# Kernel optimization log

Hardware: AMD Instinct MI355X
Metric: run time of the kernel (lower is better)

The kernel has to match this reference:

```python
import jax, jax.numpy as jnp
import numpy as np

B, S, D = 4, 2048, 1024


def setup_inputs() -> dict:
    key = jax.random.key(0)
    ks = jax.random.split(key, 7)
    s = 1.0 / np.sqrt(D)
    return {
        "x": jax.random.normal(ks[0], (B, S, D), dtype=jnp.float32),
        "Wq": jax.random.normal(ks[1], (D, D), dtype=jnp.float32) * s,
        "bq": jax.random.normal(ks[2], (D,), dtype=jnp.float32) * 0.01,
        "Wk": jax.random.normal(ks[3], (D, D), dtype=jnp.float32) * s,
        "bk": jax.random.normal(ks[4], (D,), dtype=jnp.float32) * 0.01,
        "Wv": jax.random.normal(ks[5], (D, D), dtype=jnp.float32) * s,
        "bv": jax.random.normal(ks[6], (D,), dtype=jnp.float32) * 0.01,
    }


def reference(x, Wq, bq, Wk, bk, Wv, bv):
    # x: [B, S, D]; Linear uses y = x @ W^T + b (torch convention)
    q = jnp.einsum("bsd,ed->bse", x, Wq) + bq
    k = jnp.einsum("bsd,ed->bse", x, Wk) + bk
    v = jnp.einsum("bsd,ed->bse", x, Wv) + bv
    # NOTE: original module applies softmax(q k^T) with NO 1/sqrt(d) scaling
    scores = jnp.einsum("bqd,bkd->bqk", q, k)  # [B, S, S]
    attn = jax.nn.softmax(scores, axis=-1)
    return jnp.einsum("bqk,bkd->bqd", attn, v)  # [B, S, D]
```

## Files before the change

### kernel.cpp

```cpp
#include <hip/hip_runtime.h>


#define Bb 4
#define Ss 2048
#define Dd 1024
#define Mtot 8192

typedef __bf16 bf16x8 __attribute__((ext_vector_type(8)));
typedef _Float16 f16x8 __attribute__((ext_vector_type(8)));
typedef float f32x4 __attribute__((ext_vector_type(4)));
typedef int i32x4 __attribute__((ext_vector_type(4)));
typedef signed char i8x16 __attribute__((ext_vector_type(16)));
typedef unsigned short u16;
typedef unsigned int u32;
typedef unsigned char u8;
typedef u16 u16x8 __attribute__((ext_vector_type(8)));
typedef u16 u16x4 __attribute__((ext_vector_type(4)));
typedef void __attribute__((address_space(1))) gvoid_t;
typedef void __attribute__((address_space(3))) svoid_t;

#define XC 0.0625f
#define XCI 16.f
#define XFI 4096.f
#define WC 1.953125e-3f
#define WCI 512.f
#define WFI 131072.f
#define W1S 7.62939453125e-6f
#define SM_P 1.220703125e-4f
#define SX_P 4.76837158203125e-7f
#define SY_P 1.862645149230957e-9f
#define S00 3.90625e-3f
#define S01 1.52587890625e-5f
#define S11 5.9604644775390625e-8f
#define SG00 3.814697265625e-6f
#define SG01 1.4901161193847656e-8f
#define SG11 5.820766091346741e-11f

__device__ __forceinline__ void gl_lds16(const void* g, void* l) {
  __builtin_amdgcn_global_load_lds((gvoid_t*)g, (svoid_t*)l, 16, 0, 0);
}

__device__ __forceinline__ u16 f2bf(float f) {
  u32 u = __builtin_bit_cast(u32, f);
  u = (u + 0x7FFFu + ((u >> 16) & 1u)) >> 16;
  return (u16)u;
}
__device__ __forceinline__ u16 f2h(float f) {
  return __builtin_bit_cast(u16, (_Float16)f);
}
__device__ __forceinline__ bf16x8 frag_ld(const char* p) {
  u16x8 v = *(const u16x8*)p;
  return __builtin_bit_cast(bf16x8, v);
}
__device__ __forceinline__ f16x8 frag_ld_h(const char* p) {
  u16x8 v = *(const u16x8*)p;
  return __builtin_bit_cast(f16x8, v);
}
__device__ __forceinline__ f32x4 mfma_bf16(bf16x8 a, bf16x8 b, f32x4 c) {
  return __builtin_amdgcn_mfma_f32_16x16x32_bf16(a, b, c, 0, 0, 0);
}
__device__ __forceinline__ i32x4 mfma_i8(i32x4 a, i32x4 b, i32x4 c) {
  return __builtin_amdgcn_mfma_i32_16x16x64_i8(a, b, c, 0, 0, 0);
}
__device__ __forceinline__ void dig2(float v, float cs, float ci, float fi,
                                     int& d0, int& d1) {
  float t = fminf(fmaxf(v * ci, -127.f), 127.f);
  d0 = __float2int_rn(t);
  float res = v - (float)d0 * cs;
  float u = fminf(fmaxf(res * fi, -127.f), 127.f);
  d1 = __float2int_rn(u);
}

template <int GX, int GY, int GZ>
__device__ __forceinline__ void xcd_swz(int& bx, int& by, int& bz) {
  constexpr int N = GX * GY * GZ;
  int flat = (int)blockIdx.x + GX * ((int)blockIdx.y + GY * (int)blockIdx.z);
  int s = (flat & 7) * (N >> 3) + (flat >> 3);
  bx = s & (GX - 1);
  by = (s / GX) & (GY - 1);
  bz = s / (GX * GY);
}

__device__ __forceinline__ void wait_bar_keep8() {
  asm volatile("s_waitcnt vmcnt(8)" ::: "memory");
  __builtin_amdgcn_s_barrier();
  __builtin_amdgcn_sched_barrier(0);
}
__device__ __forceinline__ void wait_bar_drain() {
  asm volatile("s_waitcnt vmcnt(0)" ::: "memory");
  __builtin_amdgcn_s_barrier();
  __builtin_amdgcn_sched_barrier(0);
}
__device__ __forceinline__ void end_bar() {
  __builtin_amdgcn_sched_barrier(0);
  __builtin_amdgcn_s_barrier();
}

template <int ROUNDS, int C>
__device__ __forceinline__ void stageF(const char* g, long row0, long ldb,
                                       long k0b, char* l, int tid) {
#pragma unroll
  for (int r = 0; r < ROUNDS; ++r) {
    int s = r * 256 + tid;
    int sub = s / (16 * C);
    int t = s % (16 * C);
    int h = t >> 6;
    int lk = (t >> 4) & 3;
    int lr = t & 15;
    gl_lds16(g + (row0 + sub * 16 + lr) * ldb + k0b + (h * 4 + lk) * 16,
             l + s * 16);
  }
}

__global__ void __launch_bounds__(256) convert_w(
    const float* __restrict__ Wq, const float* __restrict__ Wk,
    const float* __restrict__ Wv,
    u8* __restrict__ wq0, u8* __restrict__ wq1,
    u8* __restrict__ wk0, u8* __restrict__ wk1, u16* __restrict__ wvh) {
  long b = blockIdx.x;
  if (b < 2048) {
    int which = (int)(b >> 10);
    const float* src = which ? Wk : Wq;
    u8* o0 = which ? wk0 : wq0;
    u8* o1 = which ? wk1 : wq1;
    long i = (b & 1023) * 256 + threadIdx.x;
    f32x4 v = ((const f32x4*)src)[i];
    u32 p0 = 0, p1 = 0;
#pragma unroll
    for (int j = 0; j < 4; ++j) {
      int d0, d1;
      dig2(v[j], WC, WCI, WFI, d0, d1);
      p0 |= ((u32)(d0 & 255)) << (8 * j);
      p1 |= ((u32)(d1 & 255)) << (8 * j);
    }
    ((u32*)o0)[i] = p0;
    ((u32*)o1)[i] = p1;
  } else {
    long i = (b - 2048) * 256 + threadIdx.x;
    f32x4 v = ((const f32x4*)Wv)[i];
    u16x4 h;
#pragma unroll
    for (int j = 0; j < 4; ++j) h[j] = f2bf(v[j]);
    ((u16x4*)wvh)[i] = h;
  }
}

__global__ void __launch_bounds__(256) transpose_w(
    const u8* __restrict__ wq0, const u8* __restrict__ wq1,
    const u8* __restrict__ wk0, const u8* __restrict__ wk1,
    u8* __restrict__ wqT0, u8* __restrict__ wqT1,
    u8* __restrict__ wkT0, u8* __restrict__ wkT1) {
  __shared__ u8 T[64][68];
  int a = blockIdx.z;
  const u8* src = a == 0 ? wq0 : a == 1 ? wq1 : a == 2 ? wk0 : wk1;
  u8* dst = a == 0 ? wqT0 : a == 1 ? wqT1 : a == 2 ? wkT0 : wkT1;
  int bi = blockIdx.y, bj = blockIdx.x;
  int t = threadIdx.x, r = t >> 2, c4 = t & 3;
  const u32* s = (const u32*)(src + (long)(bi * 64 + r) * 1024 + bj * 64 + c4 * 16);
  u32 v0 = s[0], v1 = s[1], v2 = s[2], v3 = s[3];
  u32* trow = (u32*)&T[r][c4 * 16];
  trow[0] = v0; trow[1] = v1; trow[2] = v2; trow[3] = v3;
  __syncthreads();
  u32 o[4] = {0, 0, 0, 0};
#pragma unroll
  for (int j = 0; j < 16; ++j)
    o[j >> 2] |= ((u32)T[c4 * 16 + j][r]) << (8 * (j & 3));
  u32* d = (u32*)(dst + (long)(bj * 64 + r) * 1024 + bi * 64 + c4 * 16);
  d[0] = o[0]; d[1] = o[1]; d[2] = o[2]; d[3] = o[3];
}

__global__ void __launch_bounds__(256) gvec_kernel(
    const u8* __restrict__ wqT0, const u8* __restrict__ wqT1,
    const u8* __restrict__ wkT0, const u8* __restrict__ wkT1,
    const float* __restrict__ bq, const float* __restrict__ bk,
    float* __restrict__ gq, float* __restrict__ gk, float* __restrict__ cbuf) {
  __shared__ float sbq[1024], sbk[1024];
  int tid = threadIdx.x;
  ((f32x4*)sbq)[tid] = ((const f32x4*)bq)[tid];
  ((f32x4*)sbk)[tid] = ((const f32x4*)bk)[tid];
  __syncthreads();
  int wave = tid >> 6, lane = tid & 63;
#pragma unroll
  for (int rr = 0; rr < 2; ++rr) {
    int d = blockIdx.x * 8 + wave * 2 + rr;
    i8x16 a0 = *(const i8x16*)(wqT0 + (long)d * 1024 + lane * 16);
    i8x16 a1 = *(const i8x16*)(wqT1 + (long)d * 1024 + lane * 16);
    i8x16 c0 = *(const i8x16*)(wkT0 + (long)d * 1024 + lane * 16);
    i8x16 c1 = *(const i8x16*)(wkT1 + (long)d * 1024 + lane * 16);
    float sq = 0.f, sk = 0.f;
#pragma unroll
    for (int j = 0; j < 16; ++j) {
      sq += ((float)a0[j] * WC + (float)a1[j] * W1S) * sbk[lane * 16 + j];
      sk += ((float)c0[j] * WC + (float)c1[j] * W1S) * sbq[lane * 16 + j];
    }
#pragma unroll
    for (int off = 32; off >= 1; off >>= 1) {
      sq += __shfl_xor(sq, off);
      sk += __shfl_xor(sk, off);
    }
    if (!lane) { gq[d] = sq; gk[d] = sk; }
  }
  if (blockIdx.x == 0 && wave == 0) {
    float c = 0.f;
#pragma unroll
    for (int j = 0; j < 16; ++j) c += sbq[lane * 16 + j] * sbk[lane * 16 + j];
#pragma unroll
    for (int off = 32; off >= 1; off >>= 1) c += __shfl_xor(c, off);
    if (!lane) cbuf[0] = c;
  }
}

__global__ void __launch_bounds__(256) convert_x(
    const float* __restrict__ x, const float* __restrict__ gq,
    const float* __restrict__ gk, const float* __restrict__ cbuf,
    u16* __restrict__ xh, u8* __restrict__ xd0, u8* __restrict__ xd1,
    float* __restrict__ ubuf, float* __restrict__ wbuf) {
  long b = blockIdx.x;
  int tid = threadIdx.x;
  long i = b * 256 + tid;
  f32x4 v = ((const f32x4*)x)[i];
  u16x4 h;
  u32 p0 = 0, p1 = 0;
#pragma unroll
  for (int j = 0; j < 4; ++j) {
    h[j] = f2bf(v[j]);
    int d0, d1;
    dig2(v[j], XC, XCI, XFI, d0, d1);
    p0 |= ((u32)(d0 & 255)) << (8 * j);
    p1 |= ((u32)(d1 & 255)) << (8 * j);
  }
  ((u16x4*)xh)[i] = h;
  ((u32*)xd0)[i] = p0;
  ((u32*)xd1)[i] = p1;

  f32x4 g4 = ((const f32x4*)gq)[tid];
  f32x4 k4 = ((const f32x4*)gk)[tid];
  float pu = v[0] * g4[0] + v[1] * g4[1] + v[2] * g4[2] + v[3] * g4[3];
  float pw = v[0] * k4[0] + v[1] * k4[1] + v[2] * k4[2] + v[3] * k4[3];
#pragma unroll
  for (int off = 32; off >= 1; off >>= 1) {
    pu += __shfl_xor(pu, off);
    pw += __shfl_xor(pw, off);
  }
  __shared__ float ru[4], rw[4];
  int wave = tid >> 6, lane = tid & 63;
  if (!lane) { ru[wave] = pu; rw[wave] = pw; }
  __syncthreads();
  if (!tid) {
    ubuf[b] = ru[0] + ru[1] + ru[2] + ru[3] + cbuf[0];
    wbuf[b] = rw[0] + rw[1] + rw[2] + rw[3];
  }
}

__global__ void __launch_bounds__(256, 2) g_part(
    const u8* __restrict__ wqT0, const u8* __restrict__ wqT1,
    const u8* __restrict__ wkT0, const u8* __restrict__ wkT1,
    float* __restrict__ Gpart) {
  __shared__ char lds[65536];
  const int tid = threadIdx.x;
  const int bx = blockIdx.x, by = blockIdx.y, bz = blockIdx.z;
  const long m0 = (long)by * 128;
  const int n0 = bx * 128;
  const int k00 = bz * 256;
  const int wave = tid >> 6, lane = tid & 63;
  const int wm = wave >> 1, wn = wave & 1;
  const int lr = lane & 15, lk = lane >> 4;

  i32x4 accM[4][4] = {};
  i32x4 accX[4][4] = {};
  i32x4 accY[4][4] = {};

  auto stage = [&](char* L, int kk) {
    stageF<2, 4>((const char*)wqT0, m0, 1024, kk, L + 0, tid);
    stageF<2, 4>((const char*)wqT1, m0, 1024, kk, L + 8192, tid);
    stageF<2, 4>((const char*)wkT0, n0, 1024, kk, L + 16384, tid);
    stageF<2, 4>((const char*)wkT1, n0, 1024, kk, L + 24576, tid);
  };
  auto compute = [&](const char* L) {
    i32x4 b0[4], b1[4];
#pragma unroll
    for (int nt = 0; nt < 4; ++nt) {
      int rb = (wn * 4 + nt) * 1024 + lane * 16;
      b0[nt] = *(const i32x4*)(L + 16384 + rb);
      b1[nt] = *(const i32x4*)(L + 24576 + rb);
    }
    __builtin_amdgcn_s_setprio(1);
#pragma unroll
    for (int mt = 0; mt < 4; ++mt) {
      int ra = (wm * 4 + mt) * 1024 + lane * 16;
      i32x4 a0 = *(const i32x4*)(L + ra);
      i32x4 a1 = *(const i32x4*)(L + 8192 + ra);
#pragma unroll
      for (int nt = 0; nt < 4; ++nt) {
        accM[mt][nt] = mfma_i8(a0, b0[nt], accM[mt][nt]);
        accX[mt][nt] = mfma_i8(a0, b1[nt], accX[mt][nt]);
        accX[mt][nt] = mfma_i8(a1, b0[nt], accX[mt][nt]);
        accY[mt][nt] = mfma_i8(a1, b1[nt], accY[mt][nt]);
      }
    }
    __builtin_amdgcn_s_setprio(0);
  };

  stage(lds, k00);
  for (int t = 0; t < 3; ++t) {
    char* L = lds + (t & 1) * 32768;
    stage(lds + ((t + 1) & 1) * 32768, k00 + (t + 1) * 64);
    wait_bar_keep8();
    compute(L);
    end_bar();
  }
  {
    char* L = lds + 32768;
    wait_bar_drain();
    compute(L);
  }

#pragma unroll
  for (int mt = 0; mt < 4; ++mt)
#pragma unroll
    for (int nt = 0; nt < 4; ++nt) {
      int e = n0 + wn * 64 + nt * 16 + lr;
      int gmb = (int)m0 + wm * 64 + mt * 16 + lk * 4;
      f32x4 o;
#pragma unroll
      for (int r = 0; r < 4; ++r)
        o[r] = (float)accM[mt][nt][r] * SG00 + (float)accX[mt][nt][r] * SG01 +
               (float)accY[mt][nt][r] * SG11;
      *(f32x4*)(Gpart + ((long)bz << 20) + (long)e * 1024 + gmb) = o;
    }
}

__global__ void __launch_bounds__(256) g_reduce(const float* __restrict__ Gpart,
                                                u8* __restrict__ Gt0,
                                                u8* __restrict__ Gt1) {
  int n = blockIdx.x, tid = threadIdx.x;
  long o = (long)n * 1024 + tid * 4;
  f32x4 v = *(const f32x4*)(Gpart + o);
  f32x4 v1 = *(const f32x4*)(Gpart + (1L << 20) + o);
  f32x4 v2 = *(const f32x4*)(Gpart + (2L << 20) + o);
  f32x4 v3 = *(const f32x4*)(Gpart + (3L << 20) + o);
#pragma unroll
  for (int j = 0; j < 4; ++j) v[j] = v[j] + v1[j] + v2[j] + v3[j];
  u32 p0 = 0, p1 = 0;
#pragma unroll
  for (int j = 0; j < 4; ++j) {
    int d0, d1;
    dig2(v[j], WC, WCI, WFI, d0, d1);
    p0 |= ((u32)(d0 & 255)) << (8 * j);
    p1 |= ((u32)(d1 & 255)) << (8 * j);
  }
  ((u32*)Gt0)[n * 256 + tid] = p0;
  ((u32*)Gt1)[n * 256 + tid] = p1;
}

__global__ void __launch_bounds__(256, 2) t_gemm(
    const u8* __restrict__ xd0, const u8* __restrict__ xd1,
    const u8* __restrict__ Gt0, const u8* __restrict__ Gt1,
    u8* __restrict__ t0, u8* __restrict__ t1) {
  __shared__ char lds[65536];
  const int tid = threadIdx.x;
  int bx, by, bz;
  xcd_swz<8, 64, 1>(bx, by, bz);
  const long m0 = (long)by * 128;
  const int n0 = bx * 128;
  const int wave = tid >> 6, lane = tid & 63;
  const int wm = wave >> 1, wn = wave & 1;
  const int lr = lane & 15, lk = lane >> 4;

  i32x4 accM[4][4] = {};
  i32x4 accX[4][4] = {};
  i32x4 accY[4][4] = {};

  auto stage = [&](char* L, int kk) {
    stageF<2, 4>((const char*)xd0, m0, Dd, kk, L + 0, tid);
    stageF<2, 4>((const char*)xd1, m0, Dd, kk, L + 8192, tid);
    stageF<2, 4>((const char*)Gt0, n0, 1024, kk, L + 16384, tid);
    stageF<2, 4>((const char*)Gt1, n0, 1024, kk, L + 24576, tid);
  };
  auto compute = [&](const char* L) {
    i32x4 b0[4], b1[4];
#pragma unroll
    for (int nt = 0; nt < 4; ++nt) {
      int rb = (wn * 4 + nt) * 1024 + lane * 16;
      b0[nt] = *(const i32x4*)(L + 16384 + rb);
      b1[nt] = *(const i32x4*)(L + 24576 + rb);
    }
    __builtin_amdgcn_s_setprio(1);
#pragma unroll
    for (int mt = 0; mt < 4; ++mt) {
      int ra = (wm * 4 + mt) * 1024 + lane * 16;
      i32x4 a0 = *(const i32x4*)(L + ra);
      i32x4 a1 = *(const i32x4*)(L + 8192 + ra);
#pragma unroll
      for (int nt = 0; nt < 4; ++nt) {
        accM[mt][nt] = mfma_i8(a0, b0[nt], accM[mt][nt]);
        accX[mt][nt] = mfma_i8(a0, b1[nt], accX[mt][nt]);
        accX[mt][nt] = mfma_i8(a1, b0[nt], accX[mt][nt]);
        accY[mt][nt] = mfma_i8(a1, b1[nt], accY[mt][nt]);
      }
    }
    __builtin_amdgcn_s_setprio(0);
  };

  stage(lds, 0);
  for (int t = 0; t < Dd / 64 - 1; ++t) {
    char* L = lds + (t & 1) * 32768;
    stage(lds + ((t + 1) & 1) * 32768, (t + 1) * 64);
    wait_bar_keep8();
    compute(L);
    end_bar();
  }
  {
    char* L = lds + ((Dd / 64 - 1) & 1) * 32768;
    wait_bar_drain();
    compute(L);
  }

#pragma unroll
  for (int mt = 0; mt < 4; ++mt)
#pragma unroll
    for (int nt = 0; nt < 4; ++nt)
#pragma unroll
      for (int r = 0; r < 4; ++r) {
        long gm = m0 + wm * 64 + mt * 16 + lk * 4 + r;
        int e = n0 + wn * 64 + nt * 16 + lr;
        float v = (float)accM[mt][nt][r] * SM_P +
                  (float)accX[mt][nt][r] * SX_P +
                  (float)accY[mt][nt][r] * SY_P;
        int d0, d1;
        dig2(v, XC, XCI, XFI, d0, d1);
        long idx = gm * Dd + e;
        t0[idx] = (u8)d0;
        t1[idx] = (u8)d1;
      }
}

__global__ void __launch_bounds__(256) v_gemm(
    const u16* __restrict__ xh, const u16* __restrict__ wvh,
    const float* __restrict__ bv, u16* __restrict__ vt) {
  __shared__ char lds[65536];
  const int tid = threadIdx.x;
  int bx, by, bz;
  xcd_swz<8, 64, 1>(bx, by, bz);
  const long m0 = (long)by * 128;
  const int n0 = bx * 128;
  const int wave = tid >> 6, lane = tid & 63;
  const int wm = wave >> 1, wn = wave & 1;
  const int lr = lane & 15, lk = lane >> 4;

  f32x4 acc[4][4] = {};

  auto stage = [&](char* L, int k0) {
    stageF<4, 8>((const char*)xh, m0, (long)Dd * 2, (long)k0 * 2, L + 0, tid);
    stageF<4, 8>((const char*)wvh, n0, (long)Dd * 2, (long)k0 * 2, L + 16384, tid);
  };
  auto compute = [&](const char* L) {
    bf16x8 af[2][4], bfr[2][4];
#pragma unroll
    for (int ks = 0; ks < 2; ++ks)
#pragma unroll
      for (int i = 0; i < 4; ++i) {
        af[ks][i] = frag_ld(L + (wm * 4 + i) * 2048 + ks * 1024 + lane * 16);
        bfr[ks][i] = frag_ld(L + 16384 + (wn * 4 + i) * 2048 + ks * 1024 + lane * 16);
      }
    __builtin_amdgcn_s_setprio(1);
#pragma unroll
    for (int ks = 0; ks < 2; ++ks)
#pragma unroll
      for (int mt = 0; mt < 4; ++mt)
#pragma unroll
        for (int nt = 0; nt < 4; ++nt)
          acc[mt][nt] = mfma_bf16(af[ks][mt], bfr[ks][nt], acc[mt][nt]);
    __builtin_amdgcn_s_setprio(0);
  };

  stage(lds, 0);
  for (int t = 0; t < Dd / 64 - 1; ++t) {
    char* L = lds + (t & 1) * 32768;
    stage(lds + ((t + 1) & 1) * 32768, (t + 1) * 64);
    wait_bar_keep8();
    compute(L);
    end_bar();
  }
  {
    char* L = lds + ((Dd / 64 - 1) & 1) * 32768;
    wait_bar_drain();
    compute(L);
  }

#pragma unroll
  for (int mt = 0; mt < 4; ++mt)
#pragma unroll
    for (int nt = 0; nt < 4; ++nt)
#pragma unroll
      for (int r = 0; r < 4; ++r) {
        long gm = m0 + wm * 64 + mt * 16 + lk * 4 + r;
        int e = n0 + wn * 64 + nt * 16 + lr;
        float v = acc[mt][nt][r] + bv[e];
        long b = gm >> 11, s = gm & 2047;
        vt[(b * Dd + e) * (long)Ss + s] = f2h(v);
      }
}

__global__ void __launch_bounds__(256, 2) score_gemm(
    const u8* __restrict__ t0, const u8* __restrict__ t1,
    const u8* __restrict__ xd0, const u8* __restrict__ xd1,
    const float* __restrict__ ubuf, const float* __restrict__ wbuf,
    float* __restrict__ scores) {
  __shared__ char lds[65536];
  const int tid = threadIdx.x;
  int bx, by, bz;
  xcd_swz<16, 16, 4>(bx, by, bz);
  const int z = bz;
  const long base = (long)z * Ss * Dd;
  const long m0 = (long)by * 128;
  const int n0 = bx * 128;
  const int wave = tid >> 6, lane = tid & 63;
  const int wm = wave >> 1, wn = wave & 1;
  const int lr = lane & 15, lk = lane >> 4;

  i32x4 accM[4][4] = {};
  i32x4 accX[4][4] = {};
  i32x4 accY[4][4] = {};

  auto stage = [&](char* L, int kk) {
    stageF<2, 4>((const char*)t0 + base, m0, Dd, kk, L + 0, tid);
    stageF<2, 4>((const char*)t1 + base, m0, Dd, kk, L + 8192, tid);
    stageF<2, 4>((const char*)xd0 + base, n0, Dd, kk, L + 16384, tid);
    stageF<2, 4>((const char*)xd1 + base, n0, Dd, kk, L + 24576, tid);
  };
  auto compute = [&](const char* L) {
    i32x4 b0[4], b1[4];
#pragma unroll
    for (int nt = 0; nt < 4; ++nt) {
      int rb = (wn * 4 + nt) * 1024 + lane * 16;
      b0[nt] = *(const i32x4*)(L + 16384 + rb);
      b1[nt] = *(const i32x4*)(L + 24576 + rb);
    }
    __builtin_amdgcn_s_setprio(1);
#pragma unroll
    for (int mt = 0; mt < 4; ++mt) {
      int ra = (wm * 4 + mt) * 1024 + lane * 16;
      i32x4 a0 = *(const i32x4*)(L + ra);
      i32x4 a1 = *(const i32x4*)(L + 8192 + ra);
#pragma unroll
      for (int nt = 0; nt < 4; ++nt) {
        accM[mt][nt] = mfma_i8(a0, b0[nt], accM[mt][nt]);
        accX[mt][nt] = mfma_i8(a0, b1[nt], accX[mt][nt]);
        accX[mt][nt] = mfma_i8(a1, b0[nt], accX[mt][nt]);
        accY[mt][nt] = mfma_i8(a1, b1[nt], accY[mt][nt]);
      }
    }
    __builtin_amdgcn_s_setprio(0);
  };

  stage(lds, 0);
  for (int t = 0; t < Dd / 64 - 1; ++t) {
    char* L = lds + (t & 1) * 32768;
    stage(lds + ((t + 1) & 1) * 32768, (t + 1) * 64);
    wait_bar_keep8();
    compute(L);
    end_bar();
  }
  {
    char* L = lds + ((Dd / 64 - 1) & 1) * 32768;
    wait_bar_drain();
    compute(L);
  }

  float* srow = scores + (long)z * Ss * Ss;
#pragma unroll
  for (int mt = 0; mt < 4; ++mt)
#pragma unroll
    for (int nt = 0; nt < 4; ++nt)
#pragma unroll
      for (int r = 0; r < 4; ++r) {
        long i = m0 + wm * 64 + mt * 16 + lk * 4 + r;
        int j = n0 + wn * 64 + nt * 16 + lr;
        srow[i * Ss + j] = (float)accM[mt][nt][r] * S00 +
                           (float)accX[mt][nt][r] * S01 +
                           (float)accY[mt][nt][r] * S11 +
                           ubuf[(z << 11) + i] + wbuf[(z << 11) + j];
      }
}

__global__ void __launch_bounds__(256) softmax_rows(const float* __restrict__ scores,
                                                    u16* __restrict__ P) {
  const long r = blockIdx.x;
  const float* row = scores + r * Ss;
  u16* prow = P + r * Ss;
  const int t = threadIdx.x;
  const int wave = t >> 6, lane = t & 63;
  f32x4 v0 = ((const f32x4*)row)[t * 2];
  f32x4 v1 = ((const f32x4*)row)[t * 2 + 1];
  float a[8];
#pragma unroll
  for (int j = 0; j < 4; ++j) { a[j] = v0[j]; a[4 + j] = v1[j]; }

  float m = a[0];
#pragma unroll
  for (int j = 1; j < 8; ++j) m = fmaxf(m, a[j]);
#pragma unroll
  for (int off = 32; off >= 1; off >>= 1) m = fmaxf(m, __shfl_xor(m, off));
  __shared__ float red[4];
  if (lane == 0) red[wave] = m;
  __syncthreads();
  m = fmaxf(fmaxf(red[0], red[1]), fmaxf(red[2], red[3]));

  float e[8];
  float s = 0.f;
#pragma unroll
  for (int j = 0; j < 8; ++j) { e[j] = __expf(a[j] - m); s += e[j]; }
#pragma unroll
  for (int off = 32; off >= 1; off >>= 1) s += __shfl_xor(s, off);
  __syncthreads();
  if (lane == 0) red[wave] = s;
  __syncthreads();
  s = red[0] + red[1] + red[2] + red[3];
  float inv = 1.0f / s;

  u16x8 pk;
#pragma unroll
  for (int j = 0; j < 8; ++j) pk[j] = f2h(e[j] * inv);
  ((u16x8*)prow)[t] = pk;
}

__global__ void __launch_bounds__(256) pv_gemm(const u16* __restrict__ P,
                                               const u16* __restrict__ vt,
                                               float* __restrict__ out) {
  __shared__ char lds[65536];
  const int tid = threadIdx.x;
  int bx, by, bz;
  xcd_swz<8, 16, 4>(bx, by, bz);
  const int z = bz;
  const u16* A = P + (long)z * Ss * Ss;
  const u16* Bp = vt + (long)z * Dd * Ss;
  const long m0 = (long)by * 128;
  const int n0 = bx * 128;

  const int wave = tid >> 6, lane = tid & 63;
  const int wm = wave >> 1, wn = wave & 1;
  const int lr = lane & 15, lk = lane >> 4;

  f32x4 acc[4][4] = {};

  auto stage = [&](char* L, int k0) {
    stageF<4, 8>((const char*)A, m0, (long)Ss * 2, (long)k0 * 2, L + 0, tid);
    stageF<4, 8>((const char*)Bp, n0, (long)Ss * 2, (long)k0 * 2, L + 16384, tid);
  };
  auto compute = [&](const char* L) {
    f16x8 af[2][4], bfr[2][4];
#pragma unroll
    for (int ks = 0; ks < 2; ++ks)
#pragma unroll
      for (int i = 0; i < 4; ++i) {
        af[ks][i] = frag_ld_h(L + (wm * 4 + i) * 2048 + ks * 1024 + lane * 16);
        bfr[ks][i] = frag_ld_h(L + 16384 + (wn * 4 + i) * 2048 + ks * 1024 + lane * 16);
      }
    __builtin_amdgcn_s_setprio(1);
#pragma unroll
    for (int ks = 0; ks < 2; ++ks)
#pragma unroll
      for (int mt = 0; mt < 4; ++mt)
#pragma unroll
        for (int nt = 0; nt < 4; ++nt)
          acc[mt][nt] = __builtin_amdgcn_mfma_f32_16x16x32_f16(af[ks][mt], bfr[ks][nt], acc[mt][nt], 0, 0, 0);
    __builtin_amdgcn_s_setprio(0);
  };

  stage(lds, 0);
  for (int t = 0; t < Ss / 64 - 1; ++t) {
    char* L = lds + (t & 1) * 32768;
    stage(lds + ((t + 1) & 1) * 32768, (t + 1) * 64);
    wait_bar_keep8();
    compute(L);
    end_bar();
  }
  {
    char* L = lds + ((Ss / 64 - 1) & 1) * 32768;
    wait_bar_drain();
    compute(L);
  }

  float* orow = out + (long)z * Ss * Dd;
#pragma unroll
  for (int mt = 0; mt < 4; ++mt)
#pragma unroll
    for (int nt = 0; nt < 4; ++nt)
#pragma unroll
      for (int r = 0; r < 4; ++r) {
        long i = m0 + wm * 64 + mt * 16 + lk * 4 + r;
        int e = n0 + wn * 64 + nt * 16 + lr;
        orow[i * Dd + e] = acc[mt][nt][r];
      }
}

extern "C" void kernel_launch(void* const* d_in, const int* in_sizes, int n_in,
                              void* d_out, int out_size, void* d_ws, size_t ws_size,
                              hipStream_t stream) {
  const float* x = (const float*)d_in[0];
  const float* Wq = (const float*)d_in[1];
  const float* bq = (const float*)d_in[2];
  const float* Wk = (const float*)d_in[3];
  const float* bk = (const float*)d_in[4];
  const float* Wv = (const float*)d_in[5];
  const float* bv = (const float*)d_in[6];
  float* out = (float*)d_out;

  char* p = (char*)d_ws;
  float* scores = (float*)p;
  u16* xh = (u16*)p;
  u8* Gt0 = (u8*)p;
  u8* Gt1 = (u8*)(p + (1L << 20));
  u16* wvh = (u16*)(p + (16L << 20));
  u8* xd0 = (u8*)(p + (64L << 20));
  u8* xd1 = (u8*)(p + (72L << 20));
  u8* t0 = (u8*)(p + (80L << 20));
  u8* t1 = (u8*)(p + (88L << 20));
  u8* wq0 = (u8*)(p + (80L << 20));
  u8* wq1 = wq0 + (1L << 20);
  u8* wk0 = wq0 + (2L << 20);
  u8* wk1 = wq0 + (3L << 20);
  float* Gpart = (float*)(p + (80L << 20));
  u16* Pbuf = (u16*)(p + (96L << 20));
  u16* vt = (u16*)(p + (128L << 20));
  u8* wqT0 = (u8*)(p + (144L << 20));
  u8* wqT1 = wqT0 + (1L << 20);
  u8* wkT0 = wqT0 + (2L << 20);
  u8* wkT1 = wqT0 + (3L << 20);
  float* gq = (float*)(p + (148L << 20));
  float* gk = gq + 1024;
  float* ubuf = gq + 2048;
  float* wbuf = ubuf + 8192;
  float* cbuf = wbuf + 8192;

  convert_w<<<dim3(3072), dim3(256), 0, stream>>>(Wq, Wk, Wv, wq0, wq1, wk0, wk1, wvh);
  transpose_w<<<dim3(16, 16, 4), dim3(256), 0, stream>>>(
      wq0, wq1, wk0, wk1, wqT0, wqT1, wkT0, wkT1);
  gvec_kernel<<<dim3(128), dim3(256), 0, stream>>>(
      wqT0, wqT1, wkT0, wkT1, bq, bk, gq, gk, cbuf);
  convert_x<<<dim3(8192), dim3(256), 0, stream>>>(
      x, gq, gk, cbuf, xh, xd0, xd1, ubuf, wbuf);
  v_gemm<<<dim3(Dd / 128, Mtot / 128), dim3(256), 0, stream>>>(xh, wvh, bv, vt);
  g_part<<<dim3(8, 8, 4), dim3(256), 0, stream>>>(wqT0, wqT1, wkT0, wkT1, Gpart);
  g_reduce<<<dim3(1024), dim3(256), 0, stream>>>(Gpart, Gt0, Gt1);
  t_gemm<<<dim3(Dd / 128, Mtot / 128), dim3(256), 0, stream>>>(
      xd0, xd1, Gt0, Gt1, t0, t1);
  score_gemm<<<dim3(Ss / 128, Ss / 128, Bb), dim3(256), 0, stream>>>(
      t0, t1, xd0, xd1, ubuf, wbuf, scores);
  softmax_rows<<<dim3(Bb * Ss), dim3(256), 0, stream>>>(scores, Pbuf);
  pv_gemm<<<dim3(Dd / 128, Ss / 128, Bb), dim3(256), 0, stream>>>(Pbuf, vt, out);
}
```

Baseline: 359.4 us.

## Replace split-int8 score GEMM with single fp16 MFMA GEMM

The score GEMM used to multiply two-digit int8 splits of T and x, which took four int8 MFMAs per tile pair. It now stores T as fp16 and computes the scores with one fp16 MFMA per k-step. The x and Wv conversions and the V GEMM move from bf16 to fp16, and the xh buffer is relocated in the workspace. This cuts MFMA work and LDS staging in the score kernel. In exchange the score GEMM reads twice the bytes per element, and there is a precision risk because unscaled scores are sensitive to error in T.

```diff
diff --git a/kernel.cpp b/kernel.cpp
--- a/kernel.cpp
+++ b/kernel.cpp
@@ -6,7 +6,6 @@
 #define Dd 1024
 #define Mtot 8192
 
-typedef __bf16 bf16x8 __attribute__((ext_vector_type(8)));
 typedef _Float16 f16x8 __attribute__((ext_vector_type(8)));
 typedef float f32x4 __attribute__((ext_vector_type(4)));
 typedef int i32x4 __attribute__((ext_vector_type(4)));
@@ -29,9 +28,6 @@
 #define SM_P 1.220703125e-4f
 #define SX_P 4.76837158203125e-7f
 #define SY_P 1.862645149230957e-9f
-#define S00 3.90625e-3f
-#define S01 1.52587890625e-5f
-#define S11 5.9604644775390625e-8f
 #define SG00 3.814697265625e-6f
 #define SG01 1.4901161193847656e-8f
 #define SG11 5.820766091346741e-11f
@@ -40,24 +36,15 @@
   __builtin_amdgcn_global_load_lds((gvoid_t*)g, (svoid_t*)l, 16, 0, 0);
 }
 
-__device__ __forceinline__ u16 f2bf(float f) {
-  u32 u = __builtin_bit_cast(u32, f);
-  u = (u + 0x7FFFu + ((u >> 16) & 1u)) >> 16;
-  return (u16)u;
-}
 __device__ __forceinline__ u16 f2h(float f) {
   return __builtin_bit_cast(u16, (_Float16)f);
-}
-__device__ __forceinline__ bf16x8 frag_ld(const char* p) {
-  u16x8 v = *(const u16x8*)p;
-  return __builtin_bit_cast(bf16x8, v);
 }
 __device__ __forceinline__ f16x8 frag_ld_h(const char* p) {
   u16x8 v = *(const u16x8*)p;
   return __builtin_bit_cast(f16x8, v);
 }
-__device__ __forceinline__ f32x4 mfma_bf16(bf16x8 a, bf16x8 b, f32x4 c) {
-  return __builtin_amdgcn_mfma_f32_16x16x32_bf16(a, b, c, 0, 0, 0);
+__device__ __forceinline__ f32x4 mfma_f16(f16x8 a, f16x8 b, f32x4 c) {
+  return __builtin_amdgcn_mfma_f32_16x16x32_f16(a, b, c, 0, 0, 0);
 }
 __device__ __forceinline__ i32x4 mfma_i8(i32x4 a, i32x4 b, i32x4 c) {
   return __builtin_amdgcn_mfma_i32_16x16x64_i8(a, b, c, 0, 0, 0);
@@ -140,7 +127,7 @@
     f32x4 v = ((const f32x4*)Wv)[i];
     u16x4 h;
 #pragma unroll
-    for (int j = 0; j < 4; ++j) h[j] = f2bf(v[j]);
+    for (int j = 0; j < 4; ++j) h[j] = f2h(v[j]);
     ((u16x4*)wvh)[i] = h;
   }
 }
@@ -223,7 +210,7 @@
   u32 p0 = 0, p1 = 0;
 #pragma unroll
   for (int j = 0; j < 4; ++j) {
-    h[j] = f2bf(v[j]);
+    h[j] = f2h(v[j]);
     int d0, d1;
     dig2(v[j], XC, XCI, XFI, d0, d1);
     p0 |= ((u32)(d0 & 255)) << (8 * j);
@@ -356,7 +343,7 @@
 __global__ void __launch_bounds__(256, 2) t_gemm(
     const u8* __restrict__ xd0, const u8* __restrict__ xd1,
     const u8* __restrict__ Gt0, const u8* __restrict__ Gt1,
-    u8* __restrict__ t0, u8* __restrict__ t1) {
+    u16* __restrict__ th) {
   __shared__ char lds[65536];
   const int tid = threadIdx.x;
   int bx, by, bz;
@@ -427,11 +414,7 @@
         float v = (float)accM[mt][nt][r] * SM_P +
                   (float)accX[mt][nt][r] * SX_P +
                   (float)accY[mt][nt][r] * SY_P;
-        int d0, d1;
-        dig2(v, XC, XCI, XFI, d0, d1);
-        long idx = gm * Dd + e;
-        t0[idx] = (u8)d0;
-        t1[idx] = (u8)d1;
+        th[gm * Dd + e] = f2h(v);
       }
 }
 
@@ -455,13 +438,13 @@
     stageF<4, 8>((const char*)wvh, n0, (long)Dd * 2, (long)k0 * 2, L + 16384, tid);
   };
   auto compute = [&](const char* L) {
-    bf16x8 af[2][4], bfr[2][4];
+    f16x8 af[2][4], bfr[2][4];
 #pragma unroll
     for (int ks = 0; ks < 2; ++ks)
 #pragma unroll
       for (int i = 0; i < 4; ++i) {
-        af[ks][i] = frag_ld(L + (wm * 4 + i) * 2048 + ks * 1024 + lane * 16);
-        bfr[ks][i] = frag_ld(L + 16384 + (wn * 4 + i) * 2048 + ks * 1024 + lane * 16);
+        af[ks][i] = frag_ld_h(L + (wm * 4 + i) * 2048 + ks * 1024 + lane * 16);
+        bfr[ks][i] = frag_ld_h(L + 16384 + (wn * 4 + i) * 2048 + ks * 1024 + lane * 16);
       }
     __builtin_amdgcn_s_setprio(1);
 #pragma unroll
@@ -470,7 +453,7 @@
       for (int mt = 0; mt < 4; ++mt)
 #pragma unroll
         for (int nt = 0; nt < 4; ++nt)
-          acc[mt][nt] = mfma_bf16(af[ks][mt], bfr[ks][nt], acc[mt][nt]);
+          acc[mt][nt] = mfma_f16(af[ks][mt], bfr[ks][nt], acc[mt][nt]);
     __builtin_amdgcn_s_setprio(0);
   };
 
@@ -503,8 +486,7 @@
 }
 
 __global__ void __launch_bounds__(256, 2) score_gemm(
-    const u8* __restrict__ t0, const u8* __restrict__ t1,
-    const u8* __restrict__ xd0, const u8* __restrict__ xd1,
+    const u16* __restrict__ th, const u16* __restrict__ xh,
     const float* __restrict__ ubuf, const float* __restrict__ wbuf,
     float* __restrict__ scores) {
   __shared__ char lds[65536];
@@ -512,45 +494,36 @@
   int bx, by, bz;
   xcd_swz<16, 16, 4>(bx, by, bz);
   const int z = bz;
-  const long base = (long)z * Ss * Dd;
+  const long base = (long)z * Ss * Dd * 2;
   const long m0 = (long)by * 128;
   const int n0 = bx * 128;
   const int wave = tid >> 6, lane = tid & 63;
   const int wm = wave >> 1, wn = wave & 1;
   const int lr = lane & 15, lk = lane >> 4;
 
-  i32x4 accM[4][4] = {};
-  i32x4 accX[4][4] = {};
-  i32x4 accY[4][4] = {};
-
-  auto stage = [&](char* L, int kk) {
-    stageF<2, 4>((const char*)t0 + base, m0, Dd, kk, L + 0, tid);
-    stageF<2, 4>((const char*)t1 + base, m0, Dd, kk, L + 8192, tid);
-    stageF<2, 4>((const char*)xd0 + base, n0, Dd, kk, L + 16384, tid);
-    stageF<2, 4>((const char*)xd1 + base, n0, Dd, kk, L + 24576, tid);
+  f32x4 acc[4][4] = {};
+
+  auto stage = [&](char* L, int k0) {
+    stageF<4, 8>((const char*)th + base, m0, (long)Dd * 2, (long)k0 * 2, L + 0, tid);
+    stageF<4, 8>((const char*)xh + base, n0, (long)Dd * 2, (long)k0 * 2, L + 16384, tid);
   };
   auto compute = [&](const char* L) {
-    i32x4 b0[4], b1[4];
-#pragma unroll
-    for (int nt = 0; nt < 4; ++nt) {
-      int rb = (wn * 4 + nt) * 1024 + lane * 16;
-      b0[nt] = *(const i32x4*)(L + 16384 + rb);
-      b1[nt] = *(const i32x4*)(L + 24576 + rb);
-    }
+    f16x8 af[2][4], bfr[2][4];
+#pragma unroll
+    for (int ks = 0; ks < 2; ++ks)
+#pragma unroll
+      for (int i = 0; i < 4; ++i) {
+        af[ks][i] = frag_ld_h(L + (wm * 4 + i) * 2048 + ks * 1024 + lane * 16);
+        bfr[ks][i] = frag_ld_h(L + 16384 + (wn * 4 + i) * 2048 + ks * 1024 + lane * 16);
+      }
     __builtin_amdgcn_s_setprio(1);
 #pragma unroll
-    for (int mt = 0; mt < 4; ++mt) {
-      int ra = (wm * 4 + mt) * 1024 + lane * 16;
-      i32x4 a0 = *(const i32x4*)(L + ra);
-      i32x4 a1 = *(const i32x4*)(L + 8192 + ra);
-#pragma unroll
-      for (int nt = 0; nt < 4; ++nt) {
-        accM[mt][nt] = mfma_i8(a0, b0[nt], accM[mt][nt]);
-        accX[mt][nt] = mfma_i8(a0, b1[nt], accX[mt][nt]);
-        accX[mt][nt] = mfma_i8(a1, b0[nt], accX[mt][nt]);
-        accY[mt][nt] = mfma_i8(a1, b1[nt], accY[mt][nt]);
-      }
-    }
+    for (int ks = 0; ks < 2; ++ks)
+#pragma unroll
+      for (int mt = 0; mt < 4; ++mt)
+#pragma unroll
+        for (int nt = 0; nt < 4; ++nt)
+          acc[mt][nt] = mfma_f16(af[ks][mt], bfr[ks][nt], acc[mt][nt]);
     __builtin_amdgcn_s_setprio(0);
   };
 
@@ -577,9 +550,7 @@
       for (int r = 0; r < 4; ++r) {
         long i = m0 + wm * 64 + mt * 16 + lk * 4 + r;
         int j = n0 + wn * 64 + nt * 16 + lr;
-        srow[i * Ss + j] = (float)accM[mt][nt][r] * S00 +
-                           (float)accX[mt][nt][r] * S01 +
-                           (float)accY[mt][nt][r] * S11 +
+        srow[i * Ss + j] = acc[mt][nt][r] +
                            ubuf[(z << 11) + i] + wbuf[(z << 11) + j];
       }
 }
@@ -664,7 +635,7 @@
       for (int mt = 0; mt < 4; ++mt)
 #pragma unroll
         for (int nt = 0; nt < 4; ++nt)
-          acc[mt][nt] = __builtin_amdgcn_mfma_f32_16x16x32_f16(af[ks][mt], bfr[ks][nt], acc[mt][nt], 0, 0, 0);
+          acc[mt][nt] = mfma_f16(af[ks][mt], bfr[ks][nt], acc[mt][nt]);
     __builtin_amdgcn_s_setprio(0);
   };
 
@@ -709,20 +680,19 @@
 
   char* p = (char*)d_ws;
   float* scores = (float*)p;
-  u16* xh = (u16*)p;
   u8* Gt0 = (u8*)p;
   u8* Gt1 = (u8*)(p + (1L << 20));
   u16* wvh = (u16*)(p + (16L << 20));
   u8* xd0 = (u8*)(p + (64L << 20));
   u8* xd1 = (u8*)(p + (72L << 20));
-  u8* t0 = (u8*)(p + (80L << 20));
-  u8* t1 = (u8*)(p + (88L << 20));
+  u16* th = (u16*)(p + (80L << 20));
   u8* wq0 = (u8*)(p + (80L << 20));
   u8* wq1 = wq0 + (1L << 20);
   u8* wk0 = wq0 + (2L << 20);
   u8* wk1 = wq0 + (3L << 20);
   float* Gpart = (float*)(p + (80L << 20));
   u16* Pbuf = (u16*)(p + (96L << 20));
+  u16* xh = (u16*)(p + (96L << 20));
   u16* vt = (u16*)(p + (128L << 20));
   u8* wqT0 = (u8*)(p + (144L << 20));
   u8* wqT1 = wqT0 + (1L << 20);
@@ -745,9 +715,9 @@
   g_part<<<dim3(8, 8, 4), dim3(256), 0, stream>>>(wqT0, wqT1, wkT0, wkT1, Gpart);
   g_reduce<<<dim3(1024), dim3(256), 0, stream>>>(Gpart, Gt0, Gt1);
   t_gemm<<<dim3(Dd / 128, Mtot / 128), dim3(256), 0, stream>>>(
-      xd0, xd1, Gt0, Gt1, t0, t1);
+      xd0, xd1, Gt0, Gt1, th);
   score_gemm<<<dim3(Ss / 128, Ss / 128, Bb), dim3(256), 0, stream>>>(
-      t0, t1, xd0, xd1, ubuf, wbuf, scores);
+      th, xh, ubuf, wbuf, scores);
   softmax_rows<<<dim3(Bb * Ss), dim3(256), 0, stream>>>(scores, Pbuf);
   pv_gemm<<<dim3(Dd / 128, Ss / 128, Bb), dim3(256), 0, stream>>>(Pbuf, vt, out);
 }
```

New measurement: 352.2 us. -2.0%, faster.
